# Performance work log

Measured on AMD Instinct MI355X. Metric: run time of the kernel, lower is better.

The kernel has to match this reference:

```python
import jax, jax.numpy as jnp
import numpy as np

B = 8
NF = 64
COUNTS = [1200, 1400, 1500, 1536, 1600, 1700, 1800, 1552]  # ragged per-batch point counts
ND = 12288  # total decoder points (= sum(COUNTS))
NE = 12288  # total encoder points
LQ = 1800   # max per-batch count (padding length)
EPS = 1e-4  # scn BatchNormalization eps


def _build_geometry():
    """Random sparse 3D voxel coords per batch on a 64^3 grid; parent cells (coord//2)
    are unique by construction so the stride-2 downsample keeps one point per cell
    and Nkv == Nd with the same per-batch ordering (matches the module's slicing)."""
    rng = np.random.default_rng(0)
    coords = []
    for b, c in enumerate(COUNTS):
        cells = rng.choice(32 * 32 * 32, size=c, replace=False)
        x, y, z = cells // 1024, (cells // 32) % 32, cells % 32
        off = rng.integers(0, 2, size=(c, 3))
        pts = np.stack([x, y, z], 1) * 2 + off
        coords.append(np.concatenate([np.full((c, 1), b), pts], 1))
    coords = np.concatenate(coords, 0)  # [ND, 4] = (batch, x, y, z)
    lut = {tuple(r): i for i, r in enumerate(coords)}
    offs = np.array([[dx, dy, dz] for dx in (-1, 0, 1) for dy in (-1, 0, 1) for dz in (-1, 0, 1)])
    nbr = np.full((ND, 27), -1, np.int32)  # 3^3 submanifold rulebook
    for i, r in enumerate(coords):
        for k, o in enumerate(offs):
            j = lut.get((r[0], r[1] + o[0], r[2] + o[1], r[3] + o[2]))
            if j is not None:
                nbr[i, k] = j
    kv_nbr = np.full((ND, 8), -1, np.int32)  # stride-2 2^3 conv rulebook (1 child per cell)
    off_id = (coords[:, 1] % 2) * 4 + (coords[:, 2] % 2) * 2 + (coords[:, 3] % 2)
    kv_nbr[np.arange(ND), off_id] = np.arange(ND)
    pad_idx = np.full((B, LQ), -1, np.int32)
    unpad_idx = np.zeros(ND, np.int32)
    s = 0
    for b, c in enumerate(COUNTS):
        pad_idx[b, :c] = np.arange(s, s + c)
        unpad_idx[s:s + c] = b * LQ + np.arange(c)
        s += c
    return nbr, kv_nbr, pad_idx, unpad_idx


def setup_inputs() -> dict:
    nbr, kv_nbr, pad_idx, unpad_idx = _build_geometry()
    key = jax.random.key(0)
    ks = jax.random.split(key, 16)
    w = lambda k, i, o: jax.random.normal(k, (i, o), jnp.float32) / np.sqrt(i)
    w3 = lambda k, t, i, o: jax.random.normal(k, (t, i, o), jnp.float32) / np.sqrt(t * i)
    return {
        "x_decoder": jax.random.normal(ks[0], (ND, NF), jnp.float32),
        "x_encoder": jax.random.normal(ks[1], (NE, NF), jnp.float32),
        "Wp1": w(ks[2], NF, NF), "Wq": w(ks[3], NF, NF), "Wk": w(ks[4], NF, NF),
        "Wv": w(ks[5], NF, NF), "Wt": w(ks[6], NF, NF), "Wq1": w(ks[7], NF, NF),
        "Wk1": w(ks[8], NF, NF), "Wv1": w(ks[9], NF, NF),
        "Wdown": w3(ks[10], 8, NF, NF),
        "W3t": w3(ks[11], 27, NF, NF), "W3a": w3(ks[12], 27, NF, NF), "W3b": w3(ks[13], 27, NF, NF),
        "bn_gamma": jnp.ones((6, NF), jnp.float32),
        "bn_beta": jnp.zeros((6, NF), jnp.float32),
        "nbr": jnp.asarray(nbr), "kv_nbr": jnp.asarray(kv_nbr),
        "pad_idx": jnp.asarray(pad_idx), "unpad_idx": jnp.asarray(unpad_idx),
    }


def _bn(x, g, b):  # training-mode scn.BatchNormalization over all active points
    m = jnp.mean(x, 0)
    v = jnp.mean(jnp.square(x - m), 0)
    return (x - m) * jax.lax.rsqrt(v + EPS) * g + b


def _gconv(f, idx, W):  # rulebook sparse conv: idx [N,K] (-1 = missing), W [K,F,O]
    mask = (idx >= 0).astype(f.dtype)[..., None]
    g = f[jnp.clip(idx, 0)] * mask  # [N, K, F]
    return jnp.einsum('nkf,kfo->no', g, W)


def _pad(f, pad_idx):  # flat [N,F] -> padded [B,L,F] + validity mask [B,L]
    m = pad_idx >= 0
    return f[jnp.clip(pad_idx, 0)] * m[..., None].astype(f.dtype), m


def reference(x_decoder, x_encoder, Wp1, Wq, Wk, Wv, Wt, Wq1, Wk1, Wv1,
              Wdown, W3t, W3a, W3b, bn_gamma, bn_beta,
              nbr, kv_nbr, pad_idx, unpad_idx):
    xd = x_decoder @ Wp1                      # p1 (1x1 submanifold conv)
    q = xd @ Wq
    ke = x_encoder @ Wk
    ve = x_encoder @ Wv
    # Stage-1 cross attention. The torch loop slices queries per batch but always
    # uses the FULL encoder K/V (dk = features.T), so it equals one global attention.
    attn = jax.nn.softmax(q @ ke.T, axis=-1)  # [ND, NE], no 1/sqrt(d) scaling in source
    xr = (attn @ ve) @ Wt                     # trans_conv (1x1)
    xd = xd + _bn(xr, bn_gamma[0], bn_beta[0])  # after_norm residual add

    q1 = xd @ Wq1
    kv = _bn(_gconv(q1, kv_nbr, Wdown), bn_gamma[1], bn_beta[1])  # stride-2 conv + BN
    k1 = kv @ Wk1
    v1 = kv @ Wv1
    # Stage-2 ragged per-batch self attention (Nkv == Nd by construction).
    qp, _ = _pad(q1, pad_idx)                 # [B, LQ, NF]
    kp, mkv = _pad(k1, pad_idx)
    vp, _ = _pad(v1, pad_idx)
    s2 = jnp.einsum('blf,bmf->blm', qp, kp)
    s2 = jnp.where(mkv[:, None, :], s2, jnp.float32(-1e30))
    o = jnp.einsum('blm,bmf->blf', jax.nn.softmax(s2, axis=-1), vp)
    xr2 = o.reshape(B * LQ, NF)[unpad_idx]    # back to flat ragged layout [ND, NF]
    xr2 = _gconv(xr2, nbr, W3t)               # trans_conv1 (3^3 submanifold conv)
    xd = xd + _bn(xr2, bn_gamma[2], bn_beta[2])  # after_norm1 residual add

    # res block: BNReLU -> conv3 -> BNReLU -> conv3, add identity, BNReLU
    z = _gconv(jax.nn.relu(_bn(xd, bn_gamma[3], bn_beta[3])), nbr, W3a)
    z = _gconv(jax.nn.relu(_bn(z, bn_gamma[4], bn_beta[4])), nbr, W3b)
    return jax.nn.relu(_bn(xd + z, bn_gamma[5], bn_beta[5]))
```

## Files before the change

kernel.cpp:

```cpp
#include <hip/hip_runtime.h>

#define NPTS 12288
#define LQPAD 1800
#define LPAD2 1856
#define EPSBN 1e-4f

typedef _Float16 half8 __attribute__((ext_vector_type(8)));
typedef _Float16 half4 __attribute__((ext_vector_type(4)));
typedef float floatx4 __attribute__((ext_vector_type(4)));

__global__ __launch_bounds__(256) void wprod16(const float* __restrict__ Wp1, const float* __restrict__ Wq,
                                               float* __restrict__ Wpq) {
    __shared__ float Bs[4096];
    __shared__ float As[4][64];
    int t = threadIdx.x;
    for (int i = t; i < 4096; i += 256) Bs[i] = Wq[i];
    int r0 = blockIdx.x * 4;
    {
        int i = t >> 6, k = t & 63;
        As[i][k] = Wp1[(r0 + i) * 64 + k];
    }
    __syncthreads();
    int i = t >> 6, j = t & 63;
    float s = 0.f;
#pragma unroll
    for (int k = 0; k < 64; k++) s += As[i][k] * Bs[k * 64 + j];
    Wpq[(r0 + i) * 64 + j] = s;
}

__global__ __launch_bounds__(256) void pack_all(const float* Wp1, const float* Wpq, const float* Wk,
                                                const float* Wv, const float* Wt_, const float* Wq1,
                                                const float* Wk1, const float* Wv1, const float* Wdown,
                                                const float* W3t, const float* W3a, const float* W3b,
                                                _Float16* __restrict__ Wf) {
    int g = blockIdx.x;
    const float* src;
    if (g == 0) src = Wp1;
    else if (g == 1) src = Wpq;
    else if (g == 2) src = Wk;
    else if (g == 3) src = Wv;
    else if (g == 4) src = Wt_;
    else if (g == 5) src = Wq1;
    else if (g == 6) src = Wk1;
    else if (g == 7) src = Wv1;
    else if (g < 16) src = Wdown + (size_t)(g - 8) * 4096;
    else if (g < 43) src = W3t + (size_t)(g - 16) * 4096;
    else if (g < 70) src = W3a + (size_t)(g - 43) * 4096;
    else src = W3b + (size_t)(g - 70) * 4096;
    int t = threadIdx.x;
    int lane = t & 63, fg = t >> 6;
    int quad = lane >> 4, qi = lane & 15;
#pragma unroll
    for (int u = 0; u < 2; u++) {
        int frag = fg * 2 + u;
        int s = frag >> 2, ct = frag & 3;
        half8 v;
#pragma unroll
        for (int j = 0; j < 8; j++) v[j] = (_Float16)src[(s * 32 + quad * 8 + j) * 64 + ct * 16 + qi];
        *(half8*)(Wf + (size_t)g * 4096 + frag * 512 + lane * 8) = v;
    }
}

__device__ inline void load_split8(const float* p, half8& hi, half8& lo) {
    float4 a = *(const float4*)p;
    float4 b = *(const float4*)(p + 4);
    float v[8] = {a.x, a.y, a.z, a.w, b.x, b.y, b.z, b.w};
#pragma unroll
    for (int j = 0; j < 8; j++) {
        _Float16 h = (_Float16)v[j];
        hi[j] = h;
        lo[j] = (_Float16)(v[j] - (float)h);
    }
}

__global__ __launch_bounds__(256) void gemm_head(const float* __restrict__ xdec, const float* __restrict__ xenc,
                                                 const _Float16* __restrict__ Wf, float* __restrict__ xd,
                                                 _Float16* __restrict__ Qh, _Float16* __restrict__ Ql,
                                                 _Float16* __restrict__ Kh, _Float16* __restrict__ Vt) {
    int z = blockIdx.y;
    const float* A = (z < 2) ? xdec : xenc;
    const _Float16* Bf = Wf + (size_t)z * 4096;
    int t = threadIdx.x;
    int lane = t & 63, wv = t >> 6;
    int quad = lane >> 4, qi = lane & 15;
    int row0w = blockIdx.x * 64 + wv * 16;
    half8 ah[2], al[2];
#pragma unroll
    for (int s = 0; s < 2; s++) load_split8(A + (size_t)(row0w + qi) * 64 + s * 32 + quad * 8, ah[s], al[s]);
    floatx4 C[4];
#pragma unroll
    for (int ct = 0; ct < 4; ct++) C[ct] = floatx4{0.f, 0.f, 0.f, 0.f};
#pragma unroll
    for (int ct = 0; ct < 4; ct++)
#pragma unroll
        for (int s = 0; s < 2; s++) {
            half8 b = *(const half8*)(Bf + (s * 4 + ct) * 512 + lane * 8);
            C[ct] = __builtin_amdgcn_mfma_f32_16x16x32_f16(ah[s], b, C[ct], 0, 0, 0);
            C[ct] = __builtin_amdgcn_mfma_f32_16x16x32_f16(al[s], b, C[ct], 0, 0, 0);
        }
    int orow = row0w + quad * 4;
    if (z == 0) {
#pragma unroll
        for (int ct = 0; ct < 4; ct++)
#pragma unroll
            for (int r = 0; r < 4; r++) xd[(size_t)(orow + r) * 64 + ct * 16 + qi] = C[ct][r];
    } else if (z == 1) {
#pragma unroll
        for (int ct = 0; ct < 4; ct++)
#pragma unroll
            for (int r = 0; r < 4; r++) {
                float v = C[ct][r];
                _Float16 h = (_Float16)v;
                Qh[(size_t)(orow + r) * 64 + ct * 16 + qi] = h;
                Ql[(size_t)(orow + r) * 64 + ct * 16 + qi] = (_Float16)(v - (float)h);
            }
    } else if (z == 2) {
#pragma unroll
        for (int ct = 0; ct < 4; ct++)
#pragma unroll
            for (int r = 0; r < 4; r++) Kh[(size_t)(orow + r) * 64 + ct * 16 + qi] = (_Float16)C[ct][r];
    } else {
#pragma unroll
        for (int ct = 0; ct < 4; ct++) {
            half4 o;
#pragma unroll
            for (int r = 0; r < 4; r++) o[r] = (_Float16)C[ct][r];
            *(half4*)(Vt + (size_t)(ct * 16 + qi) * NPTS + orow) = o;
        }
    }
}

__global__ __launch_bounds__(256) void gemm_q1(const float* __restrict__ xr, float* __restrict__ xd,
                                               const _Float16* __restrict__ Bf,
                                               const float* __restrict__ stats,
                                               const float* __restrict__ gamma,
                                               const float* __restrict__ beta,
                                               _Float16* __restrict__ Oh, _Float16* __restrict__ Ol) {
    int t = threadIdx.x;
    int lane = t & 63, wv = t >> 6;
    int quad = lane >> 4, qi = lane & 15;
    int row0w = blockIdx.x * 64 + wv * 16;
    const float inv_n = 1.f / (float)NPTS;
    half8 ah[2], al[2];
#pragma unroll
    for (int s = 0; s < 2; s++) {
        size_t base = (size_t)(row0w + qi) * 64 + s * 32 + quad * 8;
        float4 xa = *(const float4*)(xr + base);
        float4 xb = *(const float4*)(xr + base + 4);
        float4 da = *(const float4*)(xd + base);
        float4 db = *(const float4*)(xd + base + 4);
        float vx[8] = {xa.x, xa.y, xa.z, xa.w, xb.x, xb.y, xb.z, xb.w};
        float vd[8] = {da.x, da.y, da.z, da.w, db.x, db.y, db.z, db.w};
        float vo[8];
#pragma unroll
        for (int j = 0; j < 8; j++) {
            int f = s * 32 + quad * 8 + j;
            float mean = stats[f] * inv_n;
            float var = stats[64 + f] * inv_n - mean * mean;
            float val = vd[j] + (vx[j] - mean) * rsqrtf(var + EPSBN) * gamma[f] + beta[f];
            vo[j] = val;
            _Float16 h = (_Float16)val;
            ah[s][j] = h;
            al[s][j] = (_Float16)(val - (float)h);
        }
        *(float4*)(xd + base) = float4{vo[0], vo[1], vo[2], vo[3]};
        *(float4*)(xd + base + 4) = float4{vo[4], vo[5], vo[6], vo[7]};
    }
    floatx4 C[4];
#pragma unroll
    for (int ct = 0; ct < 4; ct++) C[ct] = floatx4{0.f, 0.f, 0.f, 0.f};
#pragma unroll
    for (int ct = 0; ct < 4; ct++)
#pragma unroll
        for (int s = 0; s < 2; s++) {
            half8 b = *(const half8*)(Bf + (s * 4 + ct) * 512 + lane * 8);
            C[ct] = __builtin_amdgcn_mfma_f32_16x16x32_f16(ah[s], b, C[ct], 0, 0, 0);
            C[ct] = __builtin_amdgcn_mfma_f32_16x16x32_f16(al[s], b, C[ct], 0, 0, 0);
        }
    int orow = row0w + quad * 4;
#pragma unroll
    for (int ct = 0; ct < 4; ct++)
#pragma unroll
        for (int r = 0; r < 4; r++) {
            float v = C[ct][r];
            _Float16 h = (_Float16)v;
            Oh[(size_t)(orow + r) * 64 + ct * 16 + qi] = h;
            Ol[(size_t)(orow + r) * 64 + ct * 16 + qi] = (_Float16)(v - (float)h);
        }
}

__global__ __launch_bounds__(256) void gemm_kv1(const float* __restrict__ kv, const _Float16* __restrict__ Wfk,
                                                const _Float16* __restrict__ Wfv,
                                                const float* __restrict__ stats, const float* __restrict__ gamma,
                                                const float* __restrict__ beta, const int* __restrict__ unpad,
                                                _Float16* __restrict__ Kh1, _Float16* __restrict__ Vt2) {
    int y = blockIdx.y;
    int t = threadIdx.x;
    int lane = t & 63, wv = t >> 6;
    int quad = lane >> 4, qi = lane & 15;
    int row0w = blockIdx.x * 64 + wv * 16;
    const float inv_n = 1.f / (float)NPTS;
    half8 ah[2], al[2];
#pragma unroll
    for (int s = 0; s < 2; s++) {
        const float* p = kv + (size_t)(row0w + qi) * 64 + s * 32 + quad * 8;
        float4 a = *(const float4*)p;
        float4 b2 = *(const float4*)(p + 4);
        float v[8] = {a.x, a.y, a.z, a.w, b2.x, b2.y, b2.z, b2.w};
#pragma unroll
        for (int j = 0; j < 8; j++) {
            int f = s * 32 + quad * 8 + j;
            float mean = stats[f] * inv_n;
            float var = stats[64 + f] * inv_n - mean * mean;
            float val = (v[j] - mean) * rsqrtf(var + EPSBN) * gamma[f] + beta[f];
            _Float16 h = (_Float16)val;
            ah[s][j] = h;
            al[s][j] = (_Float16)(val - (float)h);
        }
    }
    const _Float16* Bf = y ? Wfv : Wfk;
    floatx4 C[4];
#pragma unroll
    for (int ct = 0; ct < 4; ct++) C[ct] = floatx4{0.f, 0.f, 0.f, 0.f};
#pragma unroll
    for (int ct = 0; ct < 4; ct++)
#pragma unroll
        for (int s = 0; s < 2; s++) {
            half8 b = *(const half8*)(Bf + (s * 4 + ct) * 512 + lane * 8);
            C[ct] = __builtin_amdgcn_mfma_f32_16x16x32_f16(ah[s], b, C[ct], 0, 0, 0);
            C[ct] = __builtin_amdgcn_mfma_f32_16x16x32_f16(al[s], b, C[ct], 0, 0, 0);
        }
    int orow = row0w + quad * 4;
    if (y == 0) {
#pragma unroll
        for (int ct = 0; ct < 4; ct++)
#pragma unroll
            for (int r = 0; r < 4; r++) Kh1[(size_t)(orow + r) * 64 + ct * 16 + qi] = (_Float16)C[ct][r];
    } else {
        int u0 = unpad[orow], u3 = unpad[orow + 3];
        int b0 = u0 / 1800, b3 = u3 / 1800;
        if (u3 == u0 + 3 && b0 == b3) {
            int p0 = u0 - b0 * 1800;
#pragma unroll
            for (int ct = 0; ct < 4; ct++) {
                half4 o;
#pragma unroll
                for (int r = 0; r < 4; r++) o[r] = (_Float16)C[ct][r];
                *(half4*)(Vt2 + ((size_t)b0 * 64 + ct * 16 + qi) * LPAD2 + p0) = o;
            }
        } else {
#pragma unroll
            for (int r = 0; r < 4; r++) {
                int u = unpad[orow + r];
                int b = u / 1800, p = u - b * 1800;
#pragma unroll
                for (int ct = 0; ct < 4; ct++)
                    Vt2[((size_t)b * 64 + ct * 16 + qi) * LPAD2 + p] = (_Float16)C[ct][r];
            }
        }
    }
}

__global__ __launch_bounds__(256) void gconv_mfma(const _Float16* __restrict__ Xh,
                                                  const int* __restrict__ idx,
                                                  const _Float16* __restrict__ Wf,
                                                  float* __restrict__ OUT, int nk,
                                                  const float* Xadd, float* stats_out) {
    __shared__ float s_sum[64], s_ss[64];
    int t = threadIdx.x;
    int lane = t & 63, wv = t >> 6;
    int quad = lane >> 4, qi = lane & 15;
    int bx = blockIdx.x;
    int row0 = (bx >> 1) * 64 + wv * 16;
    int cb = (bx & 1) * 2;
    if (stats_out) {
        if (t < 64) {
            s_sum[t] = 0.f;
            s_ss[t] = 0.f;
        }
        __syncthreads();
    }
    floatx4 Oacc[2];
#pragma unroll
    for (int u = 0; u < 2; u++) Oacc[u] = floatx4{0.f, 0.f, 0.f, 0.f};
    const int* ip = idx + (size_t)(row0 + qi) * nk;
    for (int k = 0; k < nk; k++) {
        int j = ip[k];
        half8 a0 = half8{0, 0, 0, 0, 0, 0, 0, 0};
        half8 a1 = half8{0, 0, 0, 0, 0, 0, 0, 0};
        if (j >= 0) {
            a0 = *(const half8*)(Xh + (size_t)j * 64 + quad * 8);
            a1 = *(const half8*)(Xh + (size_t)j * 64 + 32 + quad * 8);
        }
        const _Float16* wk = Wf + (size_t)k * 4096;
#pragma unroll
        for (int u = 0; u < 2; u++) {
            int ct = cb + u;
            half8 b0 = *(const half8*)(wk + ct * 512 + lane * 8);
            half8 b1 = *(const half8*)(wk + (4 + ct) * 512 + lane * 8);
            Oacc[u] = __builtin_amdgcn_mfma_f32_16x16x32_f16(a0, b0, Oacc[u], 0, 0, 0);
            Oacc[u] = __builtin_amdgcn_mfma_f32_16x16x32_f16(a1, b1, Oacc[u], 0, 0, 0);
        }
    }
    int orow = row0 + quad * 4;
#pragma unroll
    for (int u = 0; u < 2; u++) {
        int ct = cb + u;
#pragma unroll
        for (int r = 0; r < 4; r++) OUT[(size_t)(orow + r) * 64 + ct * 16 + qi] = Oacc[u][r];
    }
    if (stats_out) {
#pragma unroll
        for (int u = 0; u < 2; u++) {
            int f = (cb + u) * 16 + qi;
            float ps = 0.f, pss = 0.f;
#pragma unroll
            for (int r = 0; r < 4; r++) {
                float v = Oacc[u][r];
                if (Xadd) v += Xadd[(size_t)(orow + r) * 64 + f];
                ps += v;
                pss += v * v;
            }
            atomicAdd(&s_sum[f], ps);
            atomicAdd(&s_ss[f], pss);
        }
        __syncthreads();
        if (t < 64) {
            atomicAdd(&stats_out[t], s_sum[t]);
            atomicAdd(&stats_out[64 + t], s_ss[t]);
        }
    }
}

__global__ __launch_bounds__(256) void bn_apply(const float* __restrict__ X, const float* X2,
                                                const float* R, float* OUT, _Float16* OUT16,
                                                const float* __restrict__ stats,
                                                const float* __restrict__ gamma,
                                                const float* __restrict__ beta,
                                                float* stats_out, int n, int do_relu) {
    __shared__ float sh[2][4][64];
    int t = threadIdx.x;
    int f = t & 63, g = t >> 6;
    float inv_n = 1.f / (float)n;
    float mean = stats[f] * inv_n;
    float var = stats[64 + f] * inv_n - mean * mean;
    float rstd = rsqrtf(var + EPSBN);
    float ga = gamma[f], be = beta[f];
    float s = 0.f, ss = 0.f;
    for (int r = blockIdx.x * 4 + g; r < n; r += gridDim.x * 4) {
        size_t i = (size_t)r * 64 + f;
        float v = X[i];
        if (X2) v += X2[i];
        v = (v - mean) * rstd * ga + be;
        if (R) v += R[i];
        if (do_relu) v = fmaxf(v, 0.f);
        if (OUT) OUT[i] = v;
        if (OUT16) OUT16[i] = (_Float16)v;
        s += v;
        ss += v * v;
    }
    if (stats_out) {
        sh[0][g][f] = s;
        sh[1][g][f] = ss;
        __syncthreads();
        if (g == 0) {
            s = sh[0][0][f] + sh[0][1][f] + sh[0][2][f] + sh[0][3][f];
            ss = sh[1][0][f] + sh[1][1][f] + sh[1][2][f] + sh[1][3][f];
            atomicAdd(&stats_out[f], s);
            atomicAdd(&stats_out[64 + f], ss);
        }
    }
}

__global__ __launch_bounds__(256) void count_valid(const int* __restrict__ pad_idx, int* __restrict__ counts) {
    int b = blockIdx.x;
    int t = threadIdx.x;
    int s = 0;
    for (int i = t; i < LQPAD; i += 256) s += (pad_idx[b * LQPAD + i] >= 0) ? 1 : 0;
    for (int off = 32; off > 0; off >>= 1) s += __shfl_xor(s, off);
    if ((t & 63) == 0) atomicAdd(&counts[b], s);
}

__global__ __launch_bounds__(256, 3) void flash1_mfma(const _Float16* __restrict__ Qh,
                                                      const _Float16* __restrict__ Ql,
                                                      const _Float16* __restrict__ Kh,
                                                      const _Float16* __restrict__ Vt,
                                                      _Float16* __restrict__ Op,
                                                      float* __restrict__ Ms,
                                                      float* __restrict__ Ls) {
    __shared__ __align__(16) _Float16 KsF[16 * 512];
    __shared__ __align__(16) _Float16 VsF[16 * 512];
    __shared__ __align__(16) _Float16 PTF[4][2 * 1024];
    int t = threadIdx.x;
    int lane = t & 63, wv = t >> 6;
    int quad = lane >> 4, qi = lane & 15;
    int qb = blockIdx.x, sp = blockIdx.y;
    int q0w = qb * 128 + wv * 32;

    half8 qh[2][2], ql[2][2];
#pragma unroll
    for (int sub = 0; sub < 2; sub++)
#pragma unroll
        for (int s = 0; s < 2; s++) {
            int qrow = q0w + sub * 16 + qi;
            qh[sub][s] = *(const half8*)(Qh + (size_t)qrow * 64 + s * 32 + quad * 8);
            ql[sub][s] = *(const half8*)(Ql + (size_t)qrow * 64 + s * 32 + quad * 8);
        }
    floatx4 Oacc[2][4];
#pragma unroll
    for (int sub = 0; sub < 2; sub++)
#pragma unroll
        for (int ft = 0; ft < 4; ft++) Oacc[sub][ft] = floatx4{0.f, 0.f, 0.f, 0.f};
    float m_i[2] = {-1e30f, -1e30f}, l_i[2] = {0.f, 0.f};

    for (int it = 0; it < 12; it++) {
        int k0 = sp * 1536 + it * 128;
        __syncthreads();
#pragma unroll
        for (int u = 0; u < 8; u++) {
            int frag = wv + 4 * u;
            if (frag < 16) {
                int kt = frag >> 1, s = frag & 1;
                int key = k0 + kt * 16 + qi;
                *(half8*)(KsF + frag * 512 + lane * 8) =
                    *(const half8*)(Kh + (size_t)key * 64 + s * 32 + quad * 8);
            } else {
                int fr = frag - 16;
                int ft = fr >> 2, s = fr & 3;
                int f = ft * 16 + qi;
                *(half8*)(VsF + fr * 512 + lane * 8) =
                    *(const half8*)(Vt + (size_t)f * NPTS + k0 + s * 32 + quad * 8);
            }
        }
        __syncthreads();
#pragma unroll
        for (int ch = 0; ch < 2; ch++) {
            half8 ka[4][2];
#pragma unroll
            for (int kt = 0; kt < 4; kt++)
#pragma unroll
                for (int s = 0; s < 2; s++)
                    ka[kt][s] = *(const half8*)(KsF + ((ch * 4 + kt) * 2 + s) * 512 + lane * 8);
            floatx4 st[2][4];
#pragma unroll
            for (int sub = 0; sub < 2; sub++)
#pragma unroll
                for (int kt = 0; kt < 4; kt++) {
                    floatx4 acc = floatx4{0.f, 0.f, 0.f, 0.f};
#pragma unroll
                    for (int s = 0; s < 2; s++) {
                        acc = __builtin_amdgcn_mfma_f32_16x16x32_f16(ka[kt][s], qh[sub][s], acc, 0, 0, 0);
                        acc = __builtin_amdgcn_mfma_f32_16x16x32_f16(ka[kt][s], ql[sub][s], acc, 0, 0, 0);
                    }
                    st[sub][kt] = acc;
                }
#pragma unroll
            for (int sub = 0; sub < 2; sub++) {
                float mloc = -1e30f;
#pragma unroll
                for (int kt = 0; kt < 4; kt++)
#pragma unroll
                    for (int r = 0; r < 4; r++) mloc = fmaxf(mloc, st[sub][kt][r]);
                mloc = fmaxf(mloc, __shfl_xor(mloc, 16));
                mloc = fmaxf(mloc, __shfl_xor(mloc, 32));
                float m_new = fmaxf(m_i[sub], mloc);
                float alpha = __expf(m_i[sub] - m_new);
                float ps = 0.f;
#pragma unroll
                for (int kt = 0; kt < 4; kt++) {
                    half4 pk;
#pragma unroll
                    for (int r = 0; r < 4; r++) {
                        float p = __expf(st[sub][kt][r] - m_new);
                        ps += p;
                        pk[r] = (_Float16)p;
                    }
                    int s = kt >> 1;
                    int qd2 = (kt & 1) * 2 + (quad >> 1);
                    *(half4*)(&PTF[wv][sub * 1024 + (s * 64 + qd2 * 16 + qi) * 8 + (quad & 1) * 4]) = pk;
                }
                ps += __shfl_xor(ps, 16);
                ps += __shfl_xor(ps, 32);
                l_i[sub] = l_i[sub] * alpha + ps;
                m_i[sub] = m_new;
#pragma unroll
                for (int ft = 0; ft < 4; ft++) Oacc[sub][ft] *= alpha;
            }
            half8 pb[2][2];
#pragma unroll
            for (int sub = 0; sub < 2; sub++)
#pragma unroll
                for (int s = 0; s < 2; s++)
                    pb[sub][s] = *(const half8*)(&PTF[wv][sub * 1024 + (s * 64 + lane) * 8]);
#pragma unroll
            for (int ft = 0; ft < 4; ft++)
#pragma unroll
                for (int s = 0; s < 2; s++) {
                    half8 v = *(const half8*)(VsF + (ft * 4 + ch * 2 + s) * 512 + lane * 8);
                    Oacc[0][ft] = __builtin_amdgcn_mfma_f32_16x16x32_f16(v, pb[0][s], Oacc[0][ft], 0, 0, 0);
                    Oacc[1][ft] = __builtin_amdgcn_mfma_f32_16x16x32_f16(v, pb[1][s], Oacc[1][ft], 0, 0, 0);
                }
        }
    }
#pragma unroll
    for (int sub = 0; sub < 2; sub++) {
#pragma unroll
        for (int ft = 0; ft < 4; ft++) {
            half4 o;
#pragma unroll
            for (int r = 0; r < 4; r++) o[r] = (_Float16)Oacc[sub][ft][r];
            *(half4*)(Op + ((size_t)sp * NPTS + q0w + sub * 16 + qi) * 64 + ft * 16 + quad * 4) = o;
        }
        if (lane < 16) {
            Ms[sp * NPTS + q0w + sub * 16 + lane] = m_i[sub];
            Ls[sp * NPTS + q0w + sub * 16 + lane] = l_i[sub];
        }
    }
}

__global__ __launch_bounds__(256) void merge_gemm(const _Float16* __restrict__ Op,
                                                  const float* __restrict__ Ms, const float* __restrict__ Ls,
                                                  const _Float16* __restrict__ Wtf,
                                                  float* __restrict__ xr, float* __restrict__ stats_out) {
    __shared__ float w8[64][8];
    __shared__ float Linv[64];
    __shared__ __align__(16) _Float16 Ah[64 * 72], Al[64 * 72];
    __shared__ float s_sum[64], s_ss[64];
    int t = threadIdx.x;
    int row0 = blockIdx.x * 64;
    if (t < 64) {
        int q = row0 + t;
        float m[8], M = -1e30f;
#pragma unroll
        for (int s = 0; s < 8; s++) {
            m[s] = Ms[s * NPTS + q];
            M = fmaxf(M, m[s]);
        }
        float L = 0.f;
#pragma unroll
        for (int s = 0; s < 8; s++) {
            float w = __expf(m[s] - M);
            w8[t][s] = w;
            L += Ls[s * NPTS + q] * w;
        }
        Linv[t] = 1.f / L;
        s_sum[t] = 0.f;
        s_ss[t] = 0.f;
    }
    __syncthreads();
    for (int k = 0; k < 4; k++) {
        int i = t + k * 256;
        int qr = i >> 4, f4 = (i & 15) * 4;
        int q = row0 + qr;
        float acc[4] = {0.f, 0.f, 0.f, 0.f};
#pragma unroll
        for (int s = 0; s < 8; s++) {
            float w = w8[qr][s];
            half4 o = *(const half4*)(Op + ((size_t)s * NPTS + q) * 64 + f4);
#pragma unroll
            for (int c = 0; c < 4; c++) acc[c] += (float)o[c] * w;
        }
        float inv = Linv[qr];
#pragma unroll
        for (int c = 0; c < 4; c++) {
            float val = acc[c] * inv;
            _Float16 h = (_Float16)val;
            Ah[qr * 72 + f4 + c] = h;
            Al[qr * 72 + f4 + c] = (_Float16)(val - (float)h);
        }
    }
    __syncthreads();
    int lane = t & 63, wv = t >> 6;
    int quad = lane >> 4, qi = lane & 15;
    int rloc = wv * 16 + qi;
    half8 ah[2], al[2];
#pragma unroll
    for (int s = 0; s < 2; s++) {
        ah[s] = *(const half8*)(Ah + rloc * 72 + s * 32 + quad * 8);
        al[s] = *(const half8*)(Al + rloc * 72 + s * 32 + quad * 8);
    }
    floatx4 C[4];
#pragma unroll
    for (int ct = 0; ct < 4; ct++) C[ct] = floatx4{0.f, 0.f, 0.f, 0.f};
#pragma unroll
    for (int ct = 0; ct < 4; ct++)
#pragma unroll
        for (int s = 0; s < 2; s++) {
            half8 b = *(const half8*)(Wtf + (s * 4 + ct) * 512 + lane * 8);
            C[ct] = __builtin_amdgcn_mfma_f32_16x16x32_f16(ah[s], b, C[ct], 0, 0, 0);
            C[ct] = __builtin_amdgcn_mfma_f32_16x16x32_f16(al[s], b, C[ct], 0, 0, 0);
        }
    int orow = row0 + wv * 16 + quad * 4;
#pragma unroll
    for (int ct = 0; ct < 4; ct++) {
        int f = ct * 16 + qi;
        float ps = 0.f, pss = 0.f;
#pragma unroll
        for (int r = 0; r < 4; r++) {
            float v = C[ct][r];
            xr[(size_t)(orow + r) * 64 + f] = v;
            ps += v;
            pss += v * v;
        }
        atomicAdd(&s_sum[f], ps);
        atomicAdd(&s_ss[f], pss);
    }
    __syncthreads();
    if (t < 64) {
        atomicAdd(&stats_out[t], s_sum[t]);
        atomicAdd(&stats_out[64 + t], s_ss[t]);
    }
}

__global__ __launch_bounds__(256) void flash2_mfma(const _Float16* __restrict__ Qh,
                                                   const _Float16* __restrict__ Ql,
                                                   const _Float16* __restrict__ Kh,
                                                   const _Float16* __restrict__ Vt2,
                                                   const int* __restrict__ pad_idx,
                                                   const int* __restrict__ counts,
                                                   _Float16* __restrict__ O) {
    int b = blockIdx.y;
    int c = counts[b];
    int qb = blockIdx.x;
    if (qb * 64 >= c) return;
    __shared__ __align__(16) _Float16 KsF[8 * 512];
    __shared__ __align__(16) _Float16 VsF[8 * 512];
    __shared__ __align__(16) _Float16 PTF[4][2 * 512];
    int t = threadIdx.x;
    int lane = t & 63, wv = t >> 6;
    int quad = lane >> 4, qi = lane & 15;
    const int* prow = pad_idx + b * LQPAD;
    int p_q = qb * 64 + wv * 16 + qi;
    int flat_q = (p_q < LQPAD) ? prow[p_q] : -1;

    half8 qh[2], ql[2];
#pragma unroll
    for (int s = 0; s < 2; s++) {
        if (flat_q >= 0) {
            qh[s] = *(const half8*)(Qh + (size_t)flat_q * 64 + s * 32 + quad * 8);
            ql[s] = *(const half8*)(Ql + (size_t)flat_q * 64 + s * 32 + quad * 8);
        } else {
            qh[s] = half8{0, 0, 0, 0, 0, 0, 0, 0};
            ql[s] = half8{0, 0, 0, 0, 0, 0, 0, 0};
        }
    }
    floatx4 Oacc[4];
#pragma unroll
    for (int ft = 0; ft < 4; ft++) Oacc[ft] = floatx4{0.f, 0.f, 0.f, 0.f};
    float m_i = -1e30f, l_i = 0.f;
    const _Float16* VtB = Vt2 + (size_t)b * 64 * LPAD2;

    int nt = (c + 63) >> 6;
    for (int it = 0; it < nt; it++) {
        int k0 = it * 64;
        __syncthreads();
#pragma unroll
        for (int u = 0; u < 4; u++) {
            int frag = wv + 4 * u;
            if (frag < 8) {
                int kt = frag >> 1, s = frag & 1;
                int kp = k0 + kt * 16 + qi;
                int flat = (kp < c) ? prow[kp] : -1;
                int d0 = s * 32 + quad * 8;
                half8 kvv = half8{0, 0, 0, 0, 0, 0, 0, 0};
                if (flat >= 0) kvv = *(const half8*)(Kh + (size_t)flat * 64 + d0);
                *(half8*)(KsF + frag * 512 + lane * 8) = kvv;
            } else {
                int fr = frag - 8;
                int ft = fr >> 1, s = fr & 1;
                int f = ft * 16 + qi;
                int key = k0 + s * 32 + quad * 8;
                *(half8*)(VsF + fr * 512 + lane * 8) = *(const half8*)(VtB + f * LPAD2 + key);
            }
        }
        __syncthreads();
        floatx4 st[4];
#pragma unroll
        for (int kt = 0; kt < 4; kt++) {
            floatx4 acc = floatx4{0.f, 0.f, 0.f, 0.f};
#pragma unroll
            for (int s = 0; s < 2; s++) {
                half8 a = *(const half8*)(KsF + (kt * 2 + s) * 512 + lane * 8);
                acc = __builtin_amdgcn_mfma_f32_16x16x32_f16(a, qh[s], acc, 0, 0, 0);
                acc = __builtin_amdgcn_mfma_f32_16x16x32_f16(a, ql[s], acc, 0, 0, 0);
            }
            st[kt] = acc;
        }
        float mloc = -1e30f;
#pragma unroll
        for (int kt = 0; kt < 4; kt++)
#pragma unroll
            for (int r = 0; r < 4; r++) mloc = fmaxf(mloc, st[kt][r]);
        mloc = fmaxf(mloc, __shfl_xor(mloc, 16));
        mloc = fmaxf(mloc, __shfl_xor(mloc, 32));
        float m_new = fmaxf(m_i, mloc);
        float alpha = __expf(m_i - m_new);
        float ps = 0.f;
#pragma unroll
        for (int kt = 0; kt < 4; kt++) {
            half4 pk;
#pragma unroll
            for (int r = 0; r < 4; r++) {
                int kpos = k0 + kt * 16 + quad * 4 + r;
                float p = (kpos < c) ? __expf(st[kt][r] - m_new) : 0.f;
                ps += p;
                pk[r] = (_Float16)p;
            }
            int s = kt >> 1;
            int qd2 = (kt & 1) * 2 + (quad >> 1);
            *(half4*)(&PTF[wv][(s * 64 + qd2 * 16 + qi) * 8 + (quad & 1) * 4]) = pk;
        }
        ps += __shfl_xor(ps, 16);
        ps += __shfl_xor(ps, 32);
        l_i = l_i * alpha + ps;
        m_i = m_new;
#pragma unroll
        for (int ft = 0; ft < 4; ft++) Oacc[ft] *= alpha;
        half8 pb[2];
#pragma unroll
        for (int s = 0; s < 2; s++) pb[s] = *(const half8*)(&PTF[wv][(s * 64 + lane) * 8]);
#pragma unroll
        for (int ft = 0; ft < 4; ft++)
#pragma unroll
            for (int s = 0; s < 2; s++) {
                half8 a = *(const half8*)(VsF + (ft * 2 + s) * 512 + lane * 8);
                Oacc[ft] = __builtin_amdgcn_mfma_f32_16x16x32_f16(a, pb[s], Oacc[ft], 0, 0, 0);
            }
    }
    if (flat_q >= 0) {
        float inv = 1.f / l_i;
#pragma unroll
        for (int ft = 0; ft < 4; ft++) {
            half4 o;
#pragma unroll
            for (int r = 0; r < 4; r++) o[r] = (_Float16)(Oacc[ft][r] * inv);
            *(half4*)(O + (size_t)flat_q * 64 + ft * 16 + quad * 4) = o;
        }
    }
}

extern "C" void kernel_launch(void* const* d_in, const int* in_sizes, int n_in,
                              void* d_out, int out_size, void* d_ws, size_t ws_size,
                              hipStream_t stream) {
    const float* x_dec = (const float*)d_in[0];
    const float* x_enc = (const float*)d_in[1];
    const float* Wp1 = (const float*)d_in[2];
    const float* Wq = (const float*)d_in[3];
    const float* Wk = (const float*)d_in[4];
    const float* Wv = (const float*)d_in[5];
    const float* Wt_ = (const float*)d_in[6];
    const float* Wq1 = (const float*)d_in[7];
    const float* Wk1 = (const float*)d_in[8];
    const float* Wv1 = (const float*)d_in[9];
    const float* Wdown = (const float*)d_in[10];
    const float* W3t = (const float*)d_in[11];
    const float* W3a = (const float*)d_in[12];
    const float* W3b = (const float*)d_in[13];
    const float* bn_g = (const float*)d_in[14];
    const float* bn_b = (const float*)d_in[15];
    const int* nbr = (const int*)d_in[16];
    const int* kv_nbr = (const int*)d_in[17];
    const int* pad_idx = (const int*)d_in[18];
    const int* unpad_idx = (const int*)d_in[19];
    float* out = (float*)d_out;
    float* ws = (float*)d_ws;

    const int N = NPTS;
    const size_t BUF = (size_t)N * 64;
    float* xd = ws;
    float* slot1 = ws + BUF;
    float* slot2 = ws + 2 * BUF;
    float* slot3 = ws + 3 * BUF;
    float* slot4 = ws + 4 * BUF;
    float* slot5 = ws + 5 * BUF;
    float* slot6 = ws + 6 * BUF;
    float* slot7 = ws + 7 * BUF;
    float* slot8 = ws + 8 * BUF;
    float* arena = ws + 9 * BUF;

    float* stats = arena;
    int* counts = (int*)(arena + 768);
    float* Ms = arena + 1024;
    float* Ls = Ms + 8 * NPTS;
    _Float16* WfA = (_Float16*)(Ls + 8 * NPTS);
    float* Wpq = (float*)(WfA + (size_t)97 * 4096);

    _Float16* Oph = (_Float16*)slot1;
    _Float16* Qh = (_Float16*)slot5;
    _Float16* Ql = Qh + BUF;
    _Float16* Kh = (_Float16*)slot6;
    _Float16* Vt = Kh + BUF;
    float* kv = slot5;
    _Float16* Qh1 = (_Float16*)slot2;
    _Float16* Ql1 = Qh1 + BUF;
    _Float16* Kh1 = (_Float16*)slot6;
    _Float16* Vt2 = (_Float16*)slot1;
    _Float16* z2h = (_Float16*)slot4;
    float* xr = slot7;
    _Float16* xrh = (_Float16*)slot7;
    float* xr2 = slot8;
    float* o2 = slot8;
    _Float16* xr2h = (_Float16*)slot6;
    float* z2 = slot3;

    const _Float16* Wtf = WfA + 4 * 4096;
    const _Float16* Wq1f = WfA + 5 * 4096;
    const _Float16* Wk1f = WfA + 6 * 4096;
    const _Float16* Wv1f = WfA + 7 * 4096;
    const _Float16* Wdf = WfA + 8 * 4096;
    const _Float16* W3tf = WfA + (size_t)16 * 4096;
    const _Float16* W3af = WfA + (size_t)43 * 4096;
    const _Float16* W3bf = WfA + (size_t)70 * 4096;

    hipMemsetAsync(stats, 0, 1024 * sizeof(float), stream);

    dim3 B(256);
    int gG = N / 64;
    int gC2 = 2 * gG;

    wprod16<<<16, B, 0, stream>>>(Wp1, Wq, Wpq);
    pack_all<<<97, B, 0, stream>>>(Wp1, Wpq, Wk, Wv, Wt_, Wq1, Wk1, Wv1, Wdown, W3t, W3a, W3b, WfA);
    count_valid<<<8, B, 0, stream>>>(pad_idx, counts);

    gemm_head<<<dim3(gG, 4), B, 0, stream>>>(x_dec, x_enc, WfA, xd, Qh, Ql, Kh, Vt);
    flash1_mfma<<<dim3(N / 128, 8), B, 0, stream>>>(Qh, Ql, Kh, Vt, Oph, Ms, Ls);
    merge_gemm<<<gG, B, 0, stream>>>(Oph, Ms, Ls, Wtf, xr, stats + 0);
    gemm_q1<<<gG, B, 0, stream>>>(xr, xd, Wq1f, stats + 0, bn_g + 0, bn_b + 0, Qh1, Ql1);

    gconv_mfma<<<gC2, B, 0, stream>>>(Qh1, kv_nbr, Wdf, kv, 8, nullptr, stats + 128);
    gemm_kv1<<<dim3(gG, 2), B, 0, stream>>>(kv, Wk1f, Wv1f, stats + 128, bn_g + 64, bn_b + 64,
                                            unpad_idx, Kh1, Vt2);
    flash2_mfma<<<dim3(LPAD2 / 64, 8), B, 0, stream>>>(Qh1, Ql1, Kh1, Vt2, pad_idx, counts, z2h);
    gconv_mfma<<<gC2, B, 0, stream>>>(z2h, nbr, W3tf, xr2, 27, nullptr, stats + 256);
    bn_apply<<<256, B, 0, stream>>>(xr2, nullptr, xd, xd, nullptr, stats + 256, bn_g + 128, bn_b + 128,
                                    stats + 384, N, 0);

    bn_apply<<<256, B, 0, stream>>>(xd, nullptr, nullptr, nullptr, xrh, stats + 384, bn_g + 192,
                                    bn_b + 192, nullptr, N, 1);
    gconv_mfma<<<gC2, B, 0, stream>>>(xrh, nbr, W3af, o2, 27, nullptr, stats + 512);
    bn_apply<<<256, B, 0, stream>>>(o2, nullptr, nullptr, nullptr, xr2h, stats + 512, bn_g + 256,
                                    bn_b + 256, nullptr, N, 1);
    gconv_mfma<<<gC2, B, 0, stream>>>(xr2h, nbr, W3bf, z2, 27, xd, stats + 640);
    bn_apply<<<256, B, 0, stream>>>(xd, z2, nullptr, out, nullptr, stats + 640, bn_g + 320, bn_b + 320,
                                    nullptr, N, 1);
}
```

Before: 415.2 us.

## Drop low-half Q split in attention, shrink flash1 tiles, prefetch gconv rows

Removes the fp16 hi/lo split of Q in both attention stages, halving the QK^T MFMA count and dropping the Ql stores and loads. Flash1 now processes 64-key tiles instead of 128, using less shared memory per block. The gather convolution also prefetches the next neighbour row while the current one is being multiplied. Dropping the low-order Q term lowers the precision of the attention scores, which may push results past tolerance.

```diff
diff --git a/kernel.cpp b/kernel.cpp
--- a/kernel.cpp
+++ b/kernel.cpp
@@ -75,7 +75,7 @@
 
 __global__ __launch_bounds__(256) void gemm_head(const float* __restrict__ xdec, const float* __restrict__ xenc,
                                                  const _Float16* __restrict__ Wf, float* __restrict__ xd,
-                                                 _Float16* __restrict__ Qh, _Float16* __restrict__ Ql,
+                                                 _Float16* __restrict__ Qh,
                                                  _Float16* __restrict__ Kh, _Float16* __restrict__ Vt) {
     int z = blockIdx.y;
     const float* A = (z < 2) ? xdec : xenc;
@@ -108,12 +108,7 @@
 #pragma unroll
         for (int ct = 0; ct < 4; ct++)
 #pragma unroll
-            for (int r = 0; r < 4; r++) {
-                float v = C[ct][r];
-                _Float16 h = (_Float16)v;
-                Qh[(size_t)(orow + r) * 64 + ct * 16 + qi] = h;
-                Ql[(size_t)(orow + r) * 64 + ct * 16 + qi] = (_Float16)(v - (float)h);
-            }
+            for (int r = 0; r < 4; r++) Qh[(size_t)(orow + r) * 64 + ct * 16 + qi] = (_Float16)C[ct][r];
     } else if (z == 2) {
 #pragma unroll
         for (int ct = 0; ct < 4; ct++)
@@ -135,7 +130,7 @@
                                                const float* __restrict__ stats,
                                                const float* __restrict__ gamma,
                                                const float* __restrict__ beta,
-                                               _Float16* __restrict__ Oh, _Float16* __restrict__ Ol) {
+                                               _Float16* __restrict__ Oh) {
     int t = threadIdx.x;
     int lane = t & 63, wv = t >> 6;
     int quad = lane >> 4, qi = lane & 15;
@@ -181,12 +176,7 @@
 #pragma unroll
     for (int ct = 0; ct < 4; ct++)
 #pragma unroll
-        for (int r = 0; r < 4; r++) {
-            float v = C[ct][r];
-            _Float16 h = (_Float16)v;
-            Oh[(size_t)(orow + r) * 64 + ct * 16 + qi] = h;
-            Ol[(size_t)(orow + r) * 64 + ct * 16 + qi] = (_Float16)(v - (float)h);
-        }
+        for (int r = 0; r < 4; r++) Oh[(size_t)(orow + r) * 64 + ct * 16 + qi] = (_Float16)C[ct][r];
 }
 
 __global__ __launch_bounds__(256) void gemm_kv1(const float* __restrict__ kv, const _Float16* __restrict__ Wfk,
@@ -284,13 +274,22 @@
 #pragma unroll
     for (int u = 0; u < 2; u++) Oacc[u] = floatx4{0.f, 0.f, 0.f, 0.f};
     const int* ip = idx + (size_t)(row0 + qi) * nk;
+    int j = ip[0];
+    half8 a0 = half8{0, 0, 0, 0, 0, 0, 0, 0};
+    half8 a1 = half8{0, 0, 0, 0, 0, 0, 0, 0};
+    if (j >= 0) {
+        a0 = *(const half8*)(Xh + (size_t)j * 64 + quad * 8);
+        a1 = *(const half8*)(Xh + (size_t)j * 64 + 32 + quad * 8);
+    }
     for (int k = 0; k < nk; k++) {
-        int j = ip[k];
-        half8 a0 = half8{0, 0, 0, 0, 0, 0, 0, 0};
-        half8 a1 = half8{0, 0, 0, 0, 0, 0, 0, 0};
-        if (j >= 0) {
-            a0 = *(const half8*)(Xh + (size_t)j * 64 + quad * 8);
-            a1 = *(const half8*)(Xh + (size_t)j * 64 + 32 + quad * 8);
+        half8 n0 = half8{0, 0, 0, 0, 0, 0, 0, 0};
+        half8 n1 = half8{0, 0, 0, 0, 0, 0, 0, 0};
+        if (k + 1 < nk) {
+            int jn = ip[k + 1];
+            if (jn >= 0) {
+                n0 = *(const half8*)(Xh + (size_t)jn * 64 + quad * 8);
+                n1 = *(const half8*)(Xh + (size_t)jn * 64 + 32 + quad * 8);
+            }
         }
         const _Float16* wk = Wf + (size_t)k * 4096;
 #pragma unroll
@@ -301,6 +300,8 @@
             Oacc[u] = __builtin_amdgcn_mfma_f32_16x16x32_f16(a0, b0, Oacc[u], 0, 0, 0);
             Oacc[u] = __builtin_amdgcn_mfma_f32_16x16x32_f16(a1, b1, Oacc[u], 0, 0, 0);
         }
+        a0 = n0;
+        a1 = n1;
     }
     int orow = row0 + quad * 4;
 #pragma unroll
@@ -382,14 +383,13 @@
 }
 
 __global__ __launch_bounds__(256, 3) void flash1_mfma(const _Float16* __restrict__ Qh,
-                                                      const _Float16* __restrict__ Ql,
                                                       const _Float16* __restrict__ Kh,
                                                       const _Float16* __restrict__ Vt,
                                                       _Float16* __restrict__ Op,
                                                       float* __restrict__ Ms,
                                                       float* __restrict__ Ls) {
-    __shared__ __align__(16) _Float16 KsF[16 * 512];
-    __shared__ __align__(16) _Float16 VsF[16 * 512];
+    __shared__ __align__(16) _Float16 KsF[8 * 512];
+    __shared__ __align__(16) _Float16 VsF[8 * 512];
     __shared__ __align__(16) _Float16 PTF[4][2 * 1024];
     int t = threadIdx.x;
     int lane = t & 63, wv = t >> 6;
@@ -397,14 +397,13 @@
     int qb = blockIdx.x, sp = blockIdx.y;
     int q0w = qb * 128 + wv * 32;
 
-    half8 qh[2][2], ql[2][2];
+    half8 qh[2][2];
 #pragma unroll
     for (int sub = 0; sub < 2; sub++)
 #pragma unroll
         for (int s = 0; s < 2; s++) {
             int qrow = q0w + sub * 16 + qi;
             qh[sub][s] = *(const half8*)(Qh + (size_t)qrow * 64 + s * 32 + quad * 8);
-            ql[sub][s] = *(const half8*)(Ql + (size_t)qrow * 64 + s * 32 + quad * 8);
         }
     floatx4 Oacc[2][4];
 #pragma unroll
@@ -413,94 +412,88 @@
         for (int ft = 0; ft < 4; ft++) Oacc[sub][ft] = floatx4{0.f, 0.f, 0.f, 0.f};
     float m_i[2] = {-1e30f, -1e30f}, l_i[2] = {0.f, 0.f};
 
-    for (int it = 0; it < 12; it++) {
-        int k0 = sp * 1536 + it * 128;
+    for (int it = 0; it < 24; it++) {
+        int k0 = sp * 1536 + it * 64;
         __syncthreads();
 #pragma unroll
-        for (int u = 0; u < 8; u++) {
+        for (int u = 0; u < 4; u++) {
             int frag = wv + 4 * u;
-            if (frag < 16) {
+            if (frag < 8) {
                 int kt = frag >> 1, s = frag & 1;
                 int key = k0 + kt * 16 + qi;
                 *(half8*)(KsF + frag * 512 + lane * 8) =
                     *(const half8*)(Kh + (size_t)key * 64 + s * 32 + quad * 8);
             } else {
-                int fr = frag - 16;
-                int ft = fr >> 2, s = fr & 3;
+                int fr = frag - 8;
+                int ft = fr >> 1, s = fr & 1;
                 int f = ft * 16 + qi;
                 *(half8*)(VsF + fr * 512 + lane * 8) =
                     *(const half8*)(Vt + (size_t)f * NPTS + k0 + s * 32 + quad * 8);
             }
         }
         __syncthreads();
-#pragma unroll
-        for (int ch = 0; ch < 2; ch++) {
-            half8 ka[4][2];
+        half8 ka[4][2];
+#pragma unroll
+        for (int kt = 0; kt < 4; kt++)
+#pragma unroll
+            for (int s = 0; s < 2; s++) ka[kt][s] = *(const half8*)(KsF + (kt * 2 + s) * 512 + lane * 8);
+        floatx4 st[2][4];
+#pragma unroll
+        for (int sub = 0; sub < 2; sub++)
+#pragma unroll
+            for (int kt = 0; kt < 4; kt++) {
+                floatx4 acc = floatx4{0.f, 0.f, 0.f, 0.f};
+#pragma unroll
+                for (int s = 0; s < 2; s++)
+                    acc = __builtin_amdgcn_mfma_f32_16x16x32_f16(ka[kt][s], qh[sub][s], acc, 0, 0, 0);
+                st[sub][kt] = acc;
+            }
+#pragma unroll
+        for (int sub = 0; sub < 2; sub++) {
+            float mloc = -1e30f;
 #pragma unroll
             for (int kt = 0; kt < 4; kt++)
 #pragma unroll
-                for (int s = 0; s < 2; s++)
-                    ka[kt][s] = *(const half8*)(KsF + ((ch * 4 + kt) * 2 + s) * 512 + lane * 8);
-            floatx4 st[2][4];
-#pragma unroll
-            for (int sub = 0; sub < 2; sub++)
-#pragma unroll
-                for (int kt = 0; kt < 4; kt++) {
-                    floatx4 acc = floatx4{0.f, 0.f, 0.f, 0.f};
-#pragma unroll
-                    for (int s = 0; s < 2; s++) {
-                        acc = __builtin_amdgcn_mfma_f32_16x16x32_f16(ka[kt][s], qh[sub][s], acc, 0, 0, 0);
-                        acc = __builtin_amdgcn_mfma_f32_16x16x32_f16(ka[kt][s], ql[sub][s], acc, 0, 0, 0);
-                    }
-                    st[sub][kt] = acc;
+                for (int r = 0; r < 4; r++) mloc = fmaxf(mloc, st[sub][kt][r]);
+            mloc = fmaxf(mloc, __shfl_xor(mloc, 16));
+            mloc = fmaxf(mloc, __shfl_xor(mloc, 32));
+            float m_new = fmaxf(m_i[sub], mloc);
+            float alpha = __expf(m_i[sub] - m_new);
+            float ps = 0.f;
+#pragma unroll
+            for (int kt = 0; kt < 4; kt++) {
+                half4 pk;
+#pragma unroll
+                for (int r = 0; r < 4; r++) {
+                    float p = __expf(st[sub][kt][r] - m_new);
+                    ps += p;
+                    pk[r] = (_Float16)p;
                 }
-#pragma unroll
-            for (int sub = 0; sub < 2; sub++) {
-                float mloc = -1e30f;
-#pragma unroll
-                for (int kt = 0; kt < 4; kt++)
-#pragma unroll
-                    for (int r = 0; r < 4; r++) mloc = fmaxf(mloc, st[sub][kt][r]);
-                mloc = fmaxf(mloc, __shfl_xor(mloc, 16));
-                mloc = fmaxf(mloc, __shfl_xor(mloc, 32));
-                float m_new = fmaxf(m_i[sub], mloc);
-                float alpha = __expf(m_i[sub] - m_new);
-                float ps = 0.f;
-#pragma unroll
-                for (int kt = 0; kt < 4; kt++) {
-                    half4 pk;
-#pragma unroll
-                    for (int r = 0; r < 4; r++) {
-                        float p = __expf(st[sub][kt][r] - m_new);
-                        ps += p;
-                        pk[r] = (_Float16)p;
-                    }
-                    int s = kt >> 1;
-                    int qd2 = (kt & 1) * 2 + (quad >> 1);
-                    *(half4*)(&PTF[wv][sub * 1024 + (s * 64 + qd2 * 16 + qi) * 8 + (quad & 1) * 4]) = pk;
-                }
-                ps += __shfl_xor(ps, 16);
-                ps += __shfl_xor(ps, 32);
-                l_i[sub] = l_i[sub] * alpha + ps;
-                m_i[sub] = m_new;
-#pragma unroll
-                for (int ft = 0; ft < 4; ft++) Oacc[sub][ft] *= alpha;
-            }
-            half8 pb[2][2];
-#pragma unroll
-            for (int sub = 0; sub < 2; sub++)
-#pragma unroll
-                for (int s = 0; s < 2; s++)
-                    pb[sub][s] = *(const half8*)(&PTF[wv][sub * 1024 + (s * 64 + lane) * 8]);
-#pragma unroll
-            for (int ft = 0; ft < 4; ft++)
-#pragma unroll
-                for (int s = 0; s < 2; s++) {
-                    half8 v = *(const half8*)(VsF + (ft * 4 + ch * 2 + s) * 512 + lane * 8);
-                    Oacc[0][ft] = __builtin_amdgcn_mfma_f32_16x16x32_f16(v, pb[0][s], Oacc[0][ft], 0, 0, 0);
-                    Oacc[1][ft] = __builtin_amdgcn_mfma_f32_16x16x32_f16(v, pb[1][s], Oacc[1][ft], 0, 0, 0);
-                }
-        }
+                int s = kt >> 1;
+                int qd2 = (kt & 1) * 2 + (quad >> 1);
+                *(half4*)(&PTF[wv][sub * 1024 + (s * 64 + qd2 * 16 + qi) * 8 + (quad & 1) * 4]) = pk;
+            }
+            ps += __shfl_xor(ps, 16);
+            ps += __shfl_xor(ps, 32);
+            l_i[sub] = l_i[sub] * alpha + ps;
+            m_i[sub] = m_new;
+#pragma unroll
+            for (int ft = 0; ft < 4; ft++) Oacc[sub][ft] *= alpha;
+        }
+        half8 pb[2][2];
+#pragma unroll
+        for (int sub = 0; sub < 2; sub++)
+#pragma unroll
+            for (int s = 0; s < 2; s++)
+                pb[sub][s] = *(const half8*)(&PTF[wv][sub * 1024 + (s * 64 + lane) * 8]);
+#pragma unroll
+        for (int ft = 0; ft < 4; ft++)
+#pragma unroll
+            for (int s = 0; s < 2; s++) {
+                half8 v = *(const half8*)(VsF + (ft * 2 + s) * 512 + lane * 8);
+                Oacc[0][ft] = __builtin_amdgcn_mfma_f32_16x16x32_f16(v, pb[0][s], Oacc[0][ft], 0, 0, 0);
+                Oacc[1][ft] = __builtin_amdgcn_mfma_f32_16x16x32_f16(v, pb[1][s], Oacc[1][ft], 0, 0, 0);
+            }
     }
 #pragma unroll
     for (int sub = 0; sub < 2; sub++) {
@@ -613,7 +606,6 @@
 }
 
 __global__ __launch_bounds__(256) void flash2_mfma(const _Float16* __restrict__ Qh,
-                                                   const _Float16* __restrict__ Ql,
                                                    const _Float16* __restrict__ Kh,
                                                    const _Float16* __restrict__ Vt2,
                                                    const int* __restrict__ pad_idx,
@@ -633,16 +625,11 @@
     int p_q = qb * 64 + wv * 16 + qi;
     int flat_q = (p_q < LQPAD) ? prow[p_q] : -1;
 
-    half8 qh[2], ql[2];
+    half8 qh[2];
 #pragma unroll
     for (int s = 0; s < 2; s++) {
-        if (flat_q >= 0) {
-            qh[s] = *(const half8*)(Qh + (size_t)flat_q * 64 + s * 32 + quad * 8);
-            ql[s] = *(const half8*)(Ql + (size_t)flat_q * 64 + s * 32 + quad * 8);
-        } else {
-            qh[s] = half8{0, 0, 0, 0, 0, 0, 0, 0};
-            ql[s] = half8{0, 0, 0, 0, 0, 0, 0, 0};
-        }
+        qh[s] = (flat_q >= 0) ? *(const half8*)(Qh + (size_t)flat_q * 64 + s * 32 + quad * 8)
+                              : half8{0, 0, 0, 0, 0, 0, 0, 0};
     }
     floatx4 Oacc[4];
 #pragma unroll
@@ -682,7 +669,6 @@
             for (int s = 0; s < 2; s++) {
                 half8 a = *(const half8*)(KsF + (kt * 2 + s) * 512 + lane * 8);
                 acc = __builtin_amdgcn_mfma_f32_16x16x32_f16(a, qh[s], acc, 0, 0, 0);
-                acc = __builtin_amdgcn_mfma_f32_16x16x32_f16(a, ql[s], acc, 0, 0, 0);
             }
             st[kt] = acc;
         }
@@ -787,12 +773,10 @@
 
     _Float16* Oph = (_Float16*)slot1;
     _Float16* Qh = (_Float16*)slot5;
-    _Float16* Ql = Qh + BUF;
     _Float16* Kh = (_Float16*)slot6;
     _Float16* Vt = Kh + BUF;
     float* kv = slot5;
     _Float16* Qh1 = (_Float16*)slot2;
-    _Float16* Ql1 = Qh1 + BUF;
     _Float16* Kh1 = (_Float16*)slot6;
     _Float16* Vt2 = (_Float16*)slot1;
     _Float16* z2h = (_Float16*)slot4;
@@ -822,15 +806,15 @@
     pack_all<<<97, B, 0, stream>>>(Wp1, Wpq, Wk, Wv, Wt_, Wq1, Wk1, Wv1, Wdown, W3t, W3a, W3b, WfA);
     count_valid<<<8, B, 0, stream>>>(pad_idx, counts);
 
-    gemm_head<<<dim3(gG, 4), B, 0, stream>>>(x_dec, x_enc, WfA, xd, Qh, Ql, Kh, Vt);
-    flash1_mfma<<<dim3(N / 128, 8), B, 0, stream>>>(Qh, Ql, Kh, Vt, Oph, Ms, Ls);
+    gemm_head<<<dim3(gG, 4), B, 0, stream>>>(x_dec, x_enc, WfA, xd, Qh, Kh, Vt);
+    flash1_mfma<<<dim3(N / 128, 8), B, 0, stream>>>(Qh, Kh, Vt, Oph, Ms, Ls);
     merge_gemm<<<gG, B, 0, stream>>>(Oph, Ms, Ls, Wtf, xr, stats + 0);
-    gemm_q1<<<gG, B, 0, stream>>>(xr, xd, Wq1f, stats + 0, bn_g + 0, bn_b + 0, Qh1, Ql1);
+    gemm_q1<<<gG, B, 0, stream>>>(xr, xd, Wq1f, stats + 0, bn_g + 0, bn_b + 0, Qh1);
 
     gconv_mfma<<<gC2, B, 0, stream>>>(Qh1, kv_nbr, Wdf, kv, 8, nullptr, stats + 128);
     gemm_kv1<<<dim3(gG, 2), B, 0, stream>>>(kv, Wk1f, Wv1f, stats + 128, bn_g + 64, bn_b + 64,
                                             unpad_idx, Kh1, Vt2);
-    flash2_mfma<<<dim3(LPAD2 / 64, 8), B, 0, stream>>>(Qh1, Ql1, Kh1, Vt2, pad_idx, counts, z2h);
+    flash2_mfma<<<dim3(LPAD2 / 64, 8), B, 0, stream>>>(Qh1, Kh1, Vt2, pad_idx, counts, z2h);
     gconv_mfma<<<gC2, B, 0, stream>>>(z2h, nbr, W3tf, xr2, 27, nullptr, stats + 256);
     bn_apply<<<256, B, 0, stream>>>(xr2, nullptr, xd, xd, nullptr, stats + 256, bn_g + 128, bn_b + 128,
                                     stats + 384, N, 0);
```

Result: no change. 409.0 us (-1.5%).
